# Optimization experiments

Measured on AMD Instinct MI355X. Metric: run time of the kernel, lower is better.

The kernel has to match this reference:

```python
import jax, jax.numpy as jnp
import numpy as np


def setup_inputs() -> dict:
    key = jax.random.key(0)
    B, T, F = 128, 16384, 4
    x = jax.random.normal(key, (B, T, F), dtype=jnp.float32)
    return {"x": x, "wow": 16}


def reference(x, wow):
    # x: (B, T, F). Circular sliding-window unfold:
    # out[b, t] = concat_{k=0..wow-1} x[b, (t - wow + 1 + k) mod T, :]
    # This matches: prepend the last (wow-1) timesteps, then take every
    # length-wow window, stacked along a new axis, flattened with F.
    B, T, F = x.shape
    # idx[t, k] = (t - wow + 1 + k) mod T  -> shape (T, wow)
    idx = (jnp.arange(T)[:, None] + jnp.arange(-wow + 1, 1)[None, :]) % T
    windows = x[:, idx, :]            # (B, T, wow, F) single fused gather
    return windows.reshape(B, T, wow * F)
```

## Files before the change

kernel.cpp:

```cpp
#include <hip/hip_runtime.h>


typedef float f32x4 __attribute__((ext_vector_type(4)));

__global__ __launch_bounds__(256) void ring_pad_kernel(
    const f32x4* __restrict__ x, f32x4* __restrict__ out) {
    constexpr int T     = 16384;
    constexpr int WOW   = 16;
    constexpr int LROWS = 256 + WOW - 1;

    __shared__ f32x4 lx[LROWS];

    int b  = blockIdx.x >> 6;
    int t0 = (blockIdx.x & 63) << 8;
    int k  = threadIdx.x;

    const f32x4* xb = x + (size_t)b * T;
    lx[k] = xb[(t0 - (WOW - 1) + k) & (T - 1)];
    if (k < LROWS - 256)
        lx[k + 256] = xb[(t0 - (WOW - 1) + k + 256) & (T - 1)];
    __syncthreads();

    int w  = k & (WOW - 1);
    int tl = k >> 4;
    f32x4* ob = out + ((size_t)(b * T + t0) << 4);

    #pragma unroll
    for (int it = 0; it < 16; ++it) {
        f32x4 v = lx[it * 16 + tl + w];
        __builtin_nontemporal_store(v, &ob[it * 256 + k]);
    }
}

extern "C" void kernel_launch(void* const* d_in, const int* in_sizes, int n_in,
                              void* d_out, int out_size, void* d_ws, size_t ws_size,
                              hipStream_t stream) {
    const f32x4* x = (const f32x4*)d_in[0];
    f32x4* out = (f32x4*)d_out;

    int blocks = 128 * 64;
    ring_pad_kernel<<<blocks, 256, 0, stream>>>(x, out);
}
```

Before: 112.3 us.

## Make blocks persistent over batches with double-buffered LDS and prefetched loads

```diff
diff --git a/kernel.cpp b/kernel.cpp
--- a/kernel.cpp
+++ b/kernel.cpp
@@ -7,28 +7,40 @@
     const f32x4* __restrict__ x, f32x4* __restrict__ out) {
     constexpr int T     = 16384;
     constexpr int WOW   = 16;
-    constexpr int LROWS = 256 + WOW - 1;
+    constexpr int ROWS  = 64;
+    constexpr int LROWS = ROWS + WOW - 1;
+    constexpr int ITER  = 16;
 
-    __shared__ f32x4 lx[LROWS];
+    __shared__ f32x4 lx[2][LROWS];
 
-    int b  = blockIdx.x >> 6;
-    int t0 = (blockIdx.x & 63) << 8;
-    int k  = threadIdx.x;
+    int blk = blockIdx.x;
+    int tid = threadIdx.x;
+    int t0    = (blk & 255) * ROWS;
+    int bslab = blk >> 8;
 
-    const f32x4* xb = x + (size_t)b * T;
-    lx[k] = xb[(t0 - (WOW - 1) + k) & (T - 1)];
-    if (k < LROWS - 256)
-        lx[k + 256] = xb[(t0 - (WOW - 1) + k + 256) & (T - 1)];
-    __syncthreads();
+    int w  = tid & 15;
+    int tl = tid >> 4;
 
-    int w  = k & (WOW - 1);
-    int tl = k >> 4;
-    f32x4* ob = out + ((size_t)(b * T + t0) << 4);
+    int  srow   = (t0 - (WOW - 1) + tid) & (T - 1);
+    bool stager = tid < LROWS;
 
-    #pragma unroll
-    for (int it = 0; it < 16; ++it) {
-        f32x4 v = lx[it * 16 + tl + w];
-        __builtin_nontemporal_store(v, &ob[it * 256 + k]);
+    f32x4 r;
+    if (stager) r = x[((size_t)bslab << 14) + srow];
+
+    for (int m = 0; m < ITER; ++m) {
+        f32x4* buf = lx[m & 1];
+        if (stager) buf[tid] = r;
+        int bn = (m * 8 + 8 + bslab) & 127;
+        if (stager) r = x[((size_t)bn << 14) + srow];
+        __syncthreads();
+
+        int b = m * 8 + bslab;
+        f32x4* ob = out + ((((size_t)b << 14) + (size_t)t0) << 4);
+        #pragma unroll
+        for (int s = 0; s < 4; ++s) {
+            f32x4 v = buf[s * 16 + tl + w];
+            __builtin_nontemporal_store(v, &ob[s * 256 + tid]);
+        }
     }
 }
 
@@ -38,6 +50,5 @@
     const f32x4* x = (const f32x4*)d_in[0];
     f32x4* out = (f32x4*)d_out;
 
-    int blocks = 128 * 64;
-    ring_pad_kernel<<<blocks, 256, 0, stream>>>(x, out);
+    ring_pad_kernel<<<2048, 256, 0, stream>>>(x, out);
 }
```

After: 101.0 us. -10.1%, faster.

## Replace LDS staging with wavefront shuffles and a persistent grid-stride loop

Applied to the files above, without the earlier changes.

```diff
diff --git a/kernel.cpp b/kernel.cpp
--- a/kernel.cpp
+++ b/kernel.cpp
@@ -3,32 +3,38 @@
 
 typedef float f32x4 __attribute__((ext_vector_type(4)));
 
-__global__ __launch_bounds__(256) void ring_pad_kernel(
+__global__ __launch_bounds__(256, 8) void ring_pad_kernel(
     const f32x4* __restrict__ x, f32x4* __restrict__ out) {
-    constexpr int T     = 16384;
-    constexpr int WOW   = 16;
-    constexpr int LROWS = 256 + WOW - 1;
+    constexpr int T    = 16384;
+    constexpr int ITER = 16;
+    constexpr int NWAVE = 8192;
 
-    __shared__ f32x4 lx[LROWS];
+    int lane = threadIdx.x & 63;
+    int g = (blockIdx.x * blockDim.x + threadIdx.x) >> 6;
 
-    int b  = blockIdx.x >> 6;
-    int t0 = (blockIdx.x & 63) << 8;
-    int k  = threadIdx.x;
+    int w  = lane & 15;
+    int tl = (lane >> 4) & 3;
+    int j  = lane < 31 ? lane : 30;
 
-    const f32x4* xb = x + (size_t)b * T;
-    lx[k] = xb[(t0 - (WOW - 1) + k) & (T - 1)];
-    if (k < LROWS - 256)
-        lx[k + 256] = xb[(t0 - (WOW - 1) + k + 256) & (T - 1)];
-    __syncthreads();
+    #pragma unroll 2
+    for (int m = 0; m < ITER; ++m) {
+        int c  = m * NWAVE + g;
+        int b  = c >> 10;
+        int R0 = (c & 1023) << 4;
 
-    int w  = k & (WOW - 1);
-    int tl = k >> 4;
-    f32x4* ob = out + ((size_t)(b * T + t0) << 4);
+        f32x4 r = x[((size_t)b << 14) + ((R0 - 15 + j) & (T - 1))];
 
-    #pragma unroll
-    for (int it = 0; it < 16; ++it) {
-        f32x4 v = lx[it * 16 + tl + w];
-        __builtin_nontemporal_store(v, &ob[it * 256 + k]);
+        f32x4* ob = out + ((size_t)c << 8);
+        #pragma unroll
+        for (int s = 0; s < 4; ++s) {
+            int src = s * 4 + tl + w;
+            f32x4 v;
+            v[0] = __shfl(r[0], src, 64);
+            v[1] = __shfl(r[1], src, 64);
+            v[2] = __shfl(r[2], src, 64);
+            v[3] = __shfl(r[3], src, 64);
+            __builtin_nontemporal_store(v, &ob[s * 64 + lane]);
+        }
     }
 }
 
@@ -38,6 +44,5 @@
     const f32x4* x = (const f32x4*)d_in[0];
     f32x4* out = (f32x4*)d_out;
 
-    int blocks = 128 * 64;
-    ring_pad_kernel<<<blocks, 256, 0, stream>>>(x, out);
+    ring_pad_kernel<<<2048, 256, 0, stream>>>(x, out);
 }
```

Measured after the change: 102.1 us. -9.1%, faster.
